# Performance work log

Hardware: AMD Instinct MI355X
Metric: run time of the kernel (lower is better)

## Reference

```python
import jax, jax.numpy as jnp
import numpy as np

B, S, D = 1, 2048, 2048
NH, NKV, HD = 16, 8, 128
FF = 8192
L = 2
V = 32000
THETA = 10000.0
EPS = 1e-5
SCALE = 0.02


def setup_inputs() -> dict:
    key = jax.random.key(0)
    ks = jax.random.split(key, 16)
    return {
        "input_ids": jax.random.randint(ks[0], (B, S), 0, V, dtype=jnp.int32),
        "embed": jax.random.normal(ks[1], (V, D), jnp.float32) * SCALE,
        "Wq": jax.random.normal(ks[2], (L, D, NH * HD), jnp.float32) * SCALE,
        "Wk": jax.random.normal(ks[3], (L, D, NKV * HD), jnp.float32) * SCALE,
        "Wv": jax.random.normal(ks[4], (L, D, NKV * HD), jnp.float32) * SCALE,
        "Wo": jax.random.normal(ks[5], (L, NH * HD, D), jnp.float32) * SCALE,
        "Wgate": jax.random.normal(ks[6], (L, D, FF), jnp.float32) * SCALE,
        "Wup": jax.random.normal(ks[7], (L, D, FF), jnp.float32) * SCALE,
        "Wdown": jax.random.normal(ks[8], (L, FF, D), jnp.float32) * SCALE,
        "norm_attn": jnp.ones((L, D), jnp.float32),
        "norm_mlp": jnp.ones((L, D), jnp.float32),
        "norm_final": jnp.ones((D,), jnp.float32),
        "lm_head": jax.random.normal(ks[9], (D, V), jnp.float32) * SCALE,
        "D1": jax.random.normal(ks[10], (S,), jnp.float32) + 2.0,
        "D2": jax.random.normal(ks[11], (HD,), jnp.float32) + 2.0,
        "D3": jax.random.normal(ks[12], (S,), jnp.float32) + 2.0,
    }


def _rms_norm(x, w):
    return x * jax.lax.rsqrt(jnp.mean(x * x, axis=-1, keepdims=True) + EPS) * w


def _rotate_half(x):
    x1, x2 = jnp.split(x, 2, axis=-1)
    return jnp.concatenate([-x2, x1], axis=-1)


def _forward(input_ids, embed, Wq, Wk, Wv, Wo, Wgate, Wup, Wdown,
             norm_attn, norm_mlp, norm_final, lm_head, D1, D2, D3):
    # RoPE tables: [1,1,S,HD]
    inv_freq = 1.0 / (THETA ** (jnp.arange(0, HD, 2, dtype=jnp.float32) / HD))
    freqs = jnp.arange(S, dtype=jnp.float32)[:, None] * inv_freq[None, :]
    emb = jnp.concatenate([freqs, freqs], axis=-1)
    cos = jnp.cos(emb)[None, None]
    sin = jnp.sin(emb)[None, None]
    causal = jnp.tril(jnp.ones((S, S), dtype=bool))
    neg = jnp.finfo(jnp.float32).min
    D1i, D2i, D3i = 1.0 / D1, 1.0 / D2, 1.0 / D3
    n_rep = NH // NKV

    h = embed[input_ids]  # [B,S,D]
    for l in range(L):
        # --- attention block ---
        x = _rms_norm(h, norm_attn[l])
        q = (x @ Wq[l]).reshape(B, S, NH, HD).transpose(0, 2, 1, 3)   # [B,NH,S,HD]
        k = (x @ Wk[l]).reshape(B, S, NKV, HD).transpose(0, 2, 1, 3)  # [B,NKV,S,HD]
        v = (x @ Wv[l]).reshape(B, S, NKV, HD).transpose(0, 2, 1, 3)
        q = q * cos + _rotate_half(q) * sin
        k = k * cos + _rotate_half(k) * sin
        # repeat_kv (GQA)
        k = jnp.repeat(k, n_rep, axis=1)
        v = jnp.repeat(v, n_rep, axis=1)
        # TEE diagonal encryption: Q' = D1 Q D2, K'^T = D2^-1 K^T D3
        q_enc = q * D1[None, None, :, None] * D2[None, None, None, :]
        k_enc = k * D3[None, None, :, None] * D2i[None, None, None, :]
        scores = jnp.einsum('bhqd,bhkd->bhqk', q_enc, k_enc)
        # decrypt: D1^-1 (Q'K'^T) D3^-1  (mathematically cancels encryption)
        scores = scores * D1i[None, None, :, None] * D3i[None, None, None, :]
        scores = scores / jnp.sqrt(jnp.float32(HD))
        scores = jnp.where(causal[None, None], scores, neg)
        probs = jax.nn.softmax(scores, axis=-1)
        o = jnp.einsum('bhqk,bhkd->bhqd', probs, v)
        o = o.transpose(0, 2, 1, 3).reshape(B, S, NH * HD)
        h = h + o @ Wo[l]
        # --- SwiGLU MLP block ---
        x = _rms_norm(h, norm_mlp[l])
        h = h + (jax.nn.silu(x @ Wgate[l]) * (x @ Wup[l])) @ Wdown[l]

    h = _rms_norm(h, norm_final)
    return h @ lm_head  # logits [B,S,V]


def reference(input_ids, embed, Wq, Wk, Wv, Wo, Wgate, Wup, Wdown,
              norm_attn, norm_mlp, norm_final, lm_head, D1, D2, D3):
    return _forward(input_ids, embed, Wq, Wk, Wv, Wo, Wgate, Wup, Wdown,
                    norm_attn, norm_mlp, norm_final, lm_head, D1, D2, D3)
```

## Files before the change

### kernel.cpp

```cpp
#include <hip/hip_runtime.h>
#include <cstdint>
#include <cstddef>

typedef __attribute__((ext_vector_type(4))) float f32x4;
typedef __attribute__((ext_vector_type(8))) short short8;
typedef __attribute__((ext_vector_type(4))) unsigned int u32x4;

static const int TS = 2048;
static const int DM = 2048;
static const int NHEAD = 16, NKVH = 8, HDIM = 128;
static const int FFD = 8192;
static const int NVOC = 32000;
static const int QKVN = 4096;

__device__ __forceinline__ unsigned short f2bf(float f){
  unsigned int u = __builtin_bit_cast(unsigned int, f);
  u += 0x7FFFu + ((u >> 16) & 1u);
  return (unsigned short)(u >> 16);
}
__device__ __forceinline__ float bf2f(short h){
  unsigned int u = ((unsigned int)(unsigned short)h) << 16;
  return __builtin_bit_cast(float, u);
}
__device__ __forceinline__ f32x4 mfma16(short8 a, short8 b, f32x4 c){
  return __builtin_amdgcn_mfma_f32_16x16x32_bf16(a, b, c, 0, 0, 0);
}
__device__ __forceinline__ void gload16(const void* g, void* l){
  __builtin_amdgcn_global_load_lds(
      (const __attribute__((address_space(1))) unsigned int*)g,
      (__attribute__((address_space(3))) unsigned int*)l, 16, 0, 0);
}
__device__ __forceinline__ long toff(int r, int k, int ldk){
  return ((long)((r >> 4) * ldk + (k >> 5)) << 9)
       + (((k & 31) >> 3) << 7) + ((r & 15) << 3) + (k & 7);
}

__global__ void rope_tables_k(float* __restrict__ cosT, float* __restrict__ sinT){
  int idx = blockIdx.x * 256 + threadIdx.x;
  int s = idx >> 6, j = idx & 63;
  float inv = exp2f(-(float)j * (13.287712379549449f / 64.0f));
  float ang = (float)s * inv;
  cosT[idx] = cosf(ang);
  sinT[idx] = sinf(ang);
}

__global__ void embed_k(const int* __restrict__ ids, const float* __restrict__ E,
                        float* __restrict__ h){
  int s = blockIdx.x, tid = threadIdx.x;
  long id = ids[s];
  const f32x4* src = (const f32x4*)(E + id * (long)DM);
  f32x4* dst = (f32x4*)(h + (long)s * DM);
  dst[tid] = src[tid];
  dst[tid + 256] = src[tid + 256];
}

__global__ void rmsnorm_k(const float* __restrict__ x, const float* __restrict__ w,
                          short* __restrict__ out){
  int s = blockIdx.x, tid = threadIdx.x;
  const float* row = x + (long)s * DM;
  f32x4 v0 = *(const f32x4*)&row[tid * 8];
  f32x4 v1 = *(const f32x4*)&row[tid * 8 + 4];
  float ss = v0[0]*v0[0] + v0[1]*v0[1] + v0[2]*v0[2] + v0[3]*v0[3]
           + v1[0]*v1[0] + v1[1]*v1[1] + v1[2]*v1[2] + v1[3]*v1[3];
  #pragma unroll
  for (int off = 32; off; off >>= 1) ss += __shfl_xor(ss, off);
  __shared__ float sred[4];
  int wave = tid >> 6, lane = tid & 63;
  if (lane == 0) sred[wave] = ss;
  __syncthreads();
  float tot = sred[0] + sred[1] + sred[2] + sred[3];
  float r = rsqrtf(tot * (1.0f / (float)DM) + 1e-5f);
  f32x4 w0 = *(const f32x4*)&w[tid * 8];
  f32x4 w1 = *(const f32x4*)&w[tid * 8 + 4];
  short8 o;
  #pragma unroll
  for (int j = 0; j < 4; j++) o[j] = (short)f2bf(v0[j] * r * w0[j]);
  #pragma unroll
  for (int j = 0; j < 4; j++) o[4 + j] = (short)f2bf(v1[j] * r * w1[j]);
  *(short8*)&out[toff(s, tid * 8, DM >> 5)] = o;
}

__global__ void reduce_rms_k(const float* __restrict__ p, float* __restrict__ h,
                             const float* __restrict__ w, short* __restrict__ out){
  const long stride = (long)TS * DM;
  int s = blockIdx.x, tid = threadIdx.x;
  long i = (long)s * DM + tid * 8;
  f32x4 a0 = *(const f32x4*)&h[i];
  f32x4 a1 = *(const f32x4*)&h[i + 4];
  {
    f32x4 v0 = *(const f32x4*)&p[i];
    f32x4 v1 = *(const f32x4*)&p[i + stride];
    f32x4 v2 = *(const f32x4*)&p[i + 2 * stride];
    f32x4 v3 = *(const f32x4*)&p[i + 3 * stride];
    a0 = a0 + ((v0 + v1) + (v2 + v3));
  }
  {
    f32x4 v0 = *(const f32x4*)&p[i + 4];
    f32x4 v1 = *(const f32x4*)&p[i + 4 + stride];
    f32x4 v2 = *(const f32x4*)&p[i + 4 + 2 * stride];
    f32x4 v3 = *(const f32x4*)&p[i + 4 + 3 * stride];
    a1 = a1 + ((v0 + v1) + (v2 + v3));
  }
  *(f32x4*)&h[i] = a0;
  *(f32x4*)&h[i + 4] = a1;
  float ss = a0[0]*a0[0] + a0[1]*a0[1] + a0[2]*a0[2] + a0[3]*a0[3]
           + a1[0]*a1[0] + a1[1]*a1[1] + a1[2]*a1[2] + a1[3]*a1[3];
  #pragma unroll
  for (int off = 32; off; off >>= 1) ss += __shfl_xor(ss, off);
  __shared__ float sred[4];
  int wave = tid >> 6, lane = tid & 63;
  if (lane == 0) sred[wave] = ss;
  __syncthreads();
  float tot = sred[0] + sred[1] + sred[2] + sred[3];
  float r = rsqrtf(tot * (1.0f / (float)DM) + 1e-5f);
  f32x4 w0 = *(const f32x4*)&w[tid * 8];
  f32x4 w1 = *(const f32x4*)&w[tid * 8 + 4];
  short8 o;
  #pragma unroll
  for (int j = 0; j < 4; j++) o[j] = (short)f2bf(a0[j] * r * w0[j]);
  #pragma unroll
  for (int j = 0; j < 4; j++) o[4 + j] = (short)f2bf(a1[j] * r * w1[j]);
  *(short8*)&out[toff(s, tid * 8, DM >> 5)] = o;
}

__global__ void transpose_k(const float* __restrict__ B, short* __restrict__ Bt,
                            int K, int N){
  __shared__ float t[64][65];
  int tid = threadIdx.x;
  int kb = blockIdx.y * 64, nb = blockIdx.x * 64;
  int r0 = tid >> 4, c4 = tid & 15;
  const int ldk = K >> 5;
  #pragma unroll
  for (int p = 0; p < 4; p++){
    int r = r0 + p * 16;
    f32x4 v = *(const f32x4*)&B[(long)(kb + r) * N + nb + c4 * 4];
    t[r][c4*4+0] = v[0]; t[r][c4*4+1] = v[1]; t[r][c4*4+2] = v[2]; t[r][c4*4+3] = v[3];
  }
  __syncthreads();
  int wave = tid >> 6, lane = tid & 63;
  #pragma unroll
  for (int p = 0; p < 2; p++){
    int s = wave * 2 + p;
    int rt = s >> 1, kt = s & 1;
    int n  = rt * 16 + (lane & 15);
    int k0 = kt * 32 + (lane >> 4) * 8;
    short8 o;
    #pragma unroll
    for (int j = 0; j < 8; j++) o[j] = (short)f2bf(t[k0 + j][n]);
    long base = (((long)((nb >> 4) + rt) * ldk + (kb >> 5) + kt) << 9);
    *(short8*)&Bt[base + lane * 8] = o;
  }
}

__global__ void vtrans_k(const short* __restrict__ vb, short* __restrict__ vtb, int stride){
  int s0 = blockIdx.x * 64, kv = blockIdx.y;
  int tid = threadIdx.x;
  int s = s0 + (tid & 63);
  int d0 = (tid >> 6) * 8;
  #pragma unroll
  for (int p = 0; p < 4; p++){
    int d = d0 + p * 32;
    short8 v = *(const short8*)&vb[(long)s * stride + kv * HDIM + d];
    #pragma unroll
    for (int j = 0; j < 8; j++)
      vtb[(long)(kv * HDIM + d + j) * TS + s] = v[j];
  }
}

__global__ void rope_apply_k(short* __restrict__ buf, const float* __restrict__ cosT,
                             const float* __restrict__ sinT, int nh, int stride, int coloff){
  int idx = blockIdx.x * 256 + threadIdx.x;
  int j = idx & 63;
  int t = idx >> 6;
  int hh = t % nh;
  int s = t / nh;
  long base = (long)s * stride + coloff + hh * HDIM + j;
  float c = cosT[s * 64 + j], sn = sinT[s * 64 + j];
  float x1 = bf2f(buf[base]), x2 = bf2f(buf[base + 64]);
  buf[base]      = (short)f2bf(x1 * c - x2 * sn);
  buf[base + 64] = (short)f2bf(x2 * c + x1 * sn);
}

template<int EPI>
__global__ __launch_bounds__(512, 2)
void gemm256(const short* __restrict__ A, int ldkA,
             const short* __restrict__ Bt, int ldkB,
             float* __restrict__ Cf, short* __restrict__ Cb,
             const short* __restrict__ Xtra, int N, int K, int ldkC){
  __shared__ short lds[4][2][8192];
  const int tid = threadIdx.x;
  const int wid = tid >> 6, lane = tid & 63;
  const int wr = wid >> 2, wc = wid & 3;
  const int fr = lane & 15, fch = lane >> 4;
  const int nt = K >> 5;

  const int z = blockIdx.y;
  const int k0 = z * nt;

  const int nbt = N >> 8;
  const int nwg = nbt << 3;
  const int q = nwg >> 3;
  const int swz = (blockIdx.x & 7) * q + (blockIdx.x >> 3);
  const int mb = swz & 7, nb = swz >> 3;

  const short* Abase = A  + ((long)(mb * 16) * ldkA + k0) * 512 + lane * 8;
  const short* Bbase = Bt + ((long)(nb * 16) * ldkB + k0) * 512 + lane * 8;
  const int gA0 = wid * 2, gA1 = wid * 2 + 1;

  short8 aE[4], aO[4], bE[2], bO[2];
  f32x4 acc[8][4] = {};

#define STG_A(bufc, g_, tau_) \
  gload16(Abase + ((long)(g_) * ldkA + (tau_)) * 512, &lds[bufc][0][(g_) * 512])
#define STG_B(bufc, g_, tau_) \
  gload16(Bbase + ((long)(g_) * ldkB + (tau_)) * 512, &lds[bufc][1][(g_) * 512])
#define RDA(dst, bufc, mh) do{ \
    _Pragma("unroll") \
    for (int j_ = 0; j_ < 4; j_++) \
      dst[j_] = *(const short8*)&lds[bufc][0][(wr * 8 + (mh) * 4 + j_) * 512 + fch * 128 + fr * 8]; \
  }while(0)
#define RDB(dst, bufc, nh) do{ \
    _Pragma("unroll") \
    for (int i_ = 0; i_ < 2; i_++) \
      dst[i_] = *(const short8*)&lds[bufc][1][(wc * 4 + (nh) * 2 + i_) * 512 + fch * 128 + fr * 8]; \
  }while(0)
#define MM8(va, vb, mh, nh) do{ \
    __builtin_amdgcn_s_setprio(1); \
    _Pragma("unroll") \
    for (int j_ = 0; j_ < 4; j_++) \
      _Pragma("unroll") \
      for (int i_ = 0; i_ < 2; i_++) \
        acc[(mh)*4+j_][(nh)*2+i_] = mfma16(va[j_], vb[i_], acc[(mh)*4+j_][(nh)*2+i_]); \
    __builtin_amdgcn_s_setprio(0); \
  }while(0)
#define SB __builtin_amdgcn_sched_barrier(0)

#define TILE(t_, bufR, bufN, bufS, bC, bNx) do{ \
    const int tau_ = ((t_) + 3 < nt) ? (t_) + 3 : nt - 1; \
    RDB(bNx, bufR, 1); STG_A(bufS, gA0, tau_); SB; MM8(aE, bC, 0, 0); \
    RDA(aO,  bufR, 1); STG_A(bufS, gA1, tau_); SB; MM8(aE, bNx, 0, 1); \
    asm volatile("s_waitcnt vmcnt(6)" ::: "memory"); \
    __builtin_amdgcn_s_barrier(); \
    RDA(aE,  bufN, 0); STG_B(bufS, gA0, tau_); SB; MM8(aO, bNx, 1, 1); \
    RDB(bNx, bufN, 0); STG_B(bufS, gA1, tau_); SB; MM8(aO, bC, 1, 0); \
    __builtin_amdgcn_s_barrier(); \
  }while(0)

  STG_A(0, gA0, 0); STG_A(0, gA1, 0); STG_B(0, gA0, 0); STG_B(0, gA1, 0);
  STG_A(1, gA0, 1); STG_A(1, gA1, 1); STG_B(1, gA0, 1); STG_B(1, gA1, 1);
  STG_A(2, gA0, 2); STG_A(2, gA1, 2); STG_B(2, gA0, 2); STG_B(2, gA1, 2);
  asm volatile("s_waitcnt vmcnt(8)" ::: "memory");
  __builtin_amdgcn_s_barrier();
  RDA(aE, 0, 0); RDB(bE, 0, 0);

  const int nIter = nt >> 2;
  for (int it = 0; it < nIter; ++it){
    const int t0 = it << 2;
    TILE(t0 + 0, 0, 1, 3, bE, bO);
    TILE(t0 + 1, 1, 2, 0, bO, bE);
    TILE(t0 + 2, 2, 3, 1, bE, bO);
    TILE(t0 + 3, 3, 0, 2, bO, bE);
  }
  asm volatile("s_waitcnt vmcnt(0)" ::: "memory");

#undef STG_A
#undef STG_B
#undef RDA
#undef RDB
#undef MM8
#undef SB
#undef TILE

  const int rb0 = mb * 256 + wr * 128 + fch * 4;
  const int cb0 = nb * 256 + wc * 64 + fr;
  const long pbase = (EPI == 5) ? (long)z * ((long)TS * N) : 0;
  #pragma unroll
  for (int m = 0; m < 8; m++)
    #pragma unroll
    for (int n = 0; n < 4; n++)
      #pragma unroll
      for (int i = 0; i < 4; i++){
        const int rr = rb0 + m * 16 + i, cc = cb0 + n * 16;
        long idx = (long)rr * N + cc;
        float v = acc[m][n][i];
        if constexpr (EPI == 1) Cb[idx] = (short)f2bf(v);
        else if constexpr (EPI == 3){
          float sg = 1.0f / (1.0f + __expf(-v));
          Cb[idx] = (short)f2bf(v * sg);
        } else if constexpr (EPI == 4){
          float g = bf2f(Xtra[idx]);
          Cb[toff(rr, cc, ldkC)] = (short)f2bf(g * v);
        } else {
          Cf[pbase + idx] = v;
        }
      }
}

__device__ __forceinline__ int qoff(int r, int cB){ return r * 256 + (cB ^ ((r & 7) << 4)); }
__device__ __forceinline__ int voff(int d, int cB){ return d * 128 + (cB ^ ((d & 7) << 4)); }
__device__ __forceinline__ int poff(int r, int cB){ return r * 128 + (cB ^ ((r & 7) << 4)); }

__global__ __launch_bounds__(256)
void attn_k(const short* __restrict__ qb, const short* __restrict__ kb,
            const short* __restrict__ vtb, short* __restrict__ ob){
  __shared__ short Qs[64 * 128];
  __shared__ short Ks[64 * 128];
  __shared__ short Vt[128 * 64];
  __shared__ short Ps[64 * 64];
  const int tid = threadIdx.x, wave = tid >> 6, lane = tid & 63;
  const int head = blockIdx.y, kvh = head >> 1;
  const int qt = (head & 8) ? (31 - blockIdx.x) : blockIdx.x;
  const float scale = 0.08838834764831845f;

  {
    int r0 = tid >> 4, c16 = tid & 15;
    #pragma unroll
    for (int p = 0; p < 4; p++){
      int r = r0 + p * 16;
      u32x4 v = *(const u32x4*)&qb[(long)(qt * 64 + r) * QKVN + head * HDIM + c16 * 8];
      *(u32x4*)((char*)Qs + qoff(r, c16 * 16)) = v;
    }
  }

  float mrun[4] = {-1e30f, -1e30f, -1e30f, -1e30f};
  float lrun[4] = {0.f, 0.f, 0.f, 0.f};
  f32x4 accO[8] = {};

  for (int kt = 0; kt <= qt; kt++){
    __syncthreads();
    {
      int r0 = tid >> 4, c16 = tid & 15;
      #pragma unroll
      for (int p = 0; p < 4; p++){
        int r = r0 + p * 16;
        u32x4 v = *(const u32x4*)&kb[(long)(kt * 64 + r) * QKVN + kvh * HDIM + c16 * 8];
        *(u32x4*)((char*)Ks + qoff(r, c16 * 16)) = v;
      }
      int vr0 = tid >> 3, vc = tid & 7;
      #pragma unroll
      for (int p = 0; p < 4; p++){
        int d = vr0 + p * 32;
        u32x4 v = *(const u32x4*)&vtb[(long)(kvh * HDIM + d) * TS + kt * 64 + vc * 8];
        *(u32x4*)((char*)Vt + voff(d, vc * 16)) = v;
      }
    }
    __syncthreads();

    f32x4 sacc[4] = {};
    #pragma unroll
    for (int k4 = 0; k4 < 4; k4++){
      short8 aq = *(const short8*)((const char*)Qs +
                   qoff(wave * 16 + (lane & 15), k4 * 64 + (lane >> 4) * 16));
      #pragma unroll
      for (int n = 0; n < 4; n++){
        short8 bk = *(const short8*)((const char*)Ks +
                     qoff(n * 16 + (lane & 15), k4 * 64 + (lane >> 4) * 16));
        sacc[n] = mfma16(aq, bk, sacc[n]);
      }
    }

    const bool diag = (kt == qt);
    float mt[4] = {-1e30f, -1e30f, -1e30f, -1e30f};
    #pragma unroll
    for (int n = 0; n < 4; n++)
      #pragma unroll
      for (int i = 0; i < 4; i++){
        float v = sacc[n][i] * scale;
        if (diag){
          int rr = (lane >> 4) * 4 + i + wave * 16;
          int cc = n * 16 + (lane & 15);
          if (cc > rr) v = -1e30f;
        }
        sacc[n][i] = v;
        mt[i] = fmaxf(mt[i], v);
      }
    #pragma unroll
    for (int off = 1; off < 16; off <<= 1)
      #pragma unroll
      for (int i = 0; i < 4; i++) mt[i] = fmaxf(mt[i], __shfl_xor(mt[i], off));
    float alpha[4], rsum[4];
    #pragma unroll
    for (int i = 0; i < 4; i++){
      float mn = fmaxf(mrun[i], mt[i]);
      alpha[i] = __expf(mrun[i] - mn);
      mrun[i] = mn;
      rsum[i] = 0.f;
    }
    #pragma unroll
    for (int n = 0; n < 4; n++)
      #pragma unroll
      for (int i = 0; i < 4; i++){
        float p = __expf(sacc[n][i] - mrun[i]);
        sacc[n][i] = p;
        rsum[i] += p;
      }
    #pragma unroll
    for (int off = 1; off < 16; off <<= 1)
      #pragma unroll
      for (int i = 0; i < 4; i++) rsum[i] += __shfl_xor(rsum[i], off);
    #pragma unroll
    for (int i = 0; i < 4; i++) lrun[i] = lrun[i] * alpha[i] + rsum[i];

    #pragma unroll
    for (int n = 0; n < 4; n++)
      #pragma unroll
      for (int i = 0; i < 4; i++){
        int rr = wave * 16 + (lane >> 4) * 4 + i;
        int cc = n * 16 + (lane & 15);
        *(short*)((char*)Ps + poff(rr, cc * 2)) = (short)f2bf(sacc[n][i]);
      }

    #pragma unroll
    for (int n = 0; n < 8; n++)
      #pragma unroll
      for (int i = 0; i < 4; i++) accO[n][i] *= alpha[i];
    #pragma unroll
    for (int ks = 0; ks < 2; ks++){
      short8 ap = *(const short8*)((const char*)Ps +
                   poff(wave * 16 + (lane & 15), ks * 64 + (lane >> 4) * 16));
      #pragma unroll
      for (int n = 0; n < 8; n++){
        short8 bv = *(const short8*)((const char*)Vt +
                     voff(n * 16 + (lane & 15), ks * 64 + (lane >> 4) * 16));
        accO[n] = mfma16(ap, bv, accO[n]);
      }
    }
  }

  #pragma unroll
  for (int i = 0; i < 4; i++){
    float inv = 1.0f / lrun[i];
    int rr = qt * 64 + wave * 16 + (lane >> 4) * 4 + i;
    #pragma unroll
    for (int n = 0; n < 8; n++){
      int cc = head * HDIM + n * 16 + (lane & 15);
      ob[toff(rr, cc, DM >> 5)] = (short)f2bf(accO[n][i] * inv);
    }
  }
}

extern "C" void kernel_launch(void* const* d_in, const int* in_sizes, int n_in,
                              void* d_out, int out_size, void* d_ws, size_t ws_size,
                              hipStream_t stream){
  (void)in_sizes; (void)n_in; (void)out_size; (void)ws_size;
  const int*   ids = (const int*)d_in[0];
  const float* E   = (const float*)d_in[1];
  const float* Wq  = (const float*)d_in[2];
  const float* Wk  = (const float*)d_in[3];
  const float* Wv  = (const float*)d_in[4];
  const float* Wo  = (const float*)d_in[5];
  const float* Wg  = (const float*)d_in[6];
  const float* Wu  = (const float*)d_in[7];
  const float* Wd  = (const float*)d_in[8];
  const float* nA  = (const float*)d_in[9];
  const float* nM  = (const float*)d_in[10];
  const float* nF  = (const float*)d_in[11];
  const float* LMH = (const float*)d_in[12];
  float* out = (float*)d_out;

  char* ws = (char*)d_ws;
  size_t off = 0;
  auto alloc = [&](size_t bytes){ void* p = ws + off; off += (bytes + 255) & ~(size_t)255; return p; };
  float* h    = (float*)alloc((size_t)TS * DM * 4);
  short* xb   = (short*)alloc((size_t)TS * DM * 2);
  short* qkvb = (short*)alloc((size_t)TS * QKVN * 2);
  short* vtb  = (short*)alloc((size_t)NKVH * HDIM * TS * 2);
  short* obuf = (short*)alloc((size_t)TS * DM * 2);
  short* sg   = (short*)alloc((size_t)TS * FFD * 2);
  short* actb = (short*)alloc((size_t)TS * FFD * 2);
  float* cosT = (float*)alloc((size_t)TS * 64 * 4);
  float* sinT = (float*)alloc((size_t)TS * 64 * 4);
  short* wT   = (short*)alloc((size_t)NVOC * DM * 2);
  float* pPart = (float*)((char*)wT + (size_t)36 * 1024 * 1024);

  rope_tables_k<<<512, 256, 0, stream>>>(cosT, sinT);
  embed_k<<<TS, 256, 0, stream>>>(ids, E, h);
  rmsnorm_k<<<TS, 256, 0, stream>>>(h, nA, xb);

  for (int l = 0; l < 2; l++){
    transpose_k<<<dim3(32, 32), 256, 0, stream>>>(Wq + (size_t)l * DM * DM, wT, DM, DM);
    transpose_k<<<dim3(16, 32), 256, 0, stream>>>(Wk + (size_t)l * DM * 1024, wT + (size_t)2048 * DM, DM, 1024);
    transpose_k<<<dim3(16, 32), 256, 0, stream>>>(Wv + (size_t)l * DM * 1024, wT + (size_t)3072 * DM, DM, 1024);
    gemm256<1><<<dim3(128), 512, 0, stream>>>(xb, 64, wT, 64, nullptr, qkvb, nullptr, QKVN, DM, 0);
    rope_apply_k<<<8192, 256, 0, stream>>>(qkvb, cosT, sinT, NHEAD, QKVN, 0);
    rope_apply_k<<<4096, 256, 0, stream>>>(qkvb, cosT, sinT, NKVH, QKVN, 2048);
    vtrans_k<<<dim3(32, 8), 256, 0, stream>>>(qkvb + 3072, vtb, QKVN);
    attn_k<<<dim3(32, 16), 256, 0, stream>>>(qkvb, qkvb + 2048, vtb, obuf);
    transpose_k<<<dim3(32, 32), 256, 0, stream>>>(Wo + (size_t)l * DM * DM, wT, DM, DM);
    gemm256<5><<<dim3(64, 4), 512, 0, stream>>>(obuf, 64, wT, 64, pPart, nullptr, nullptr, DM, DM / 4, 0);
    reduce_rms_k<<<TS, 256, 0, stream>>>(pPart, h, nM + (size_t)l * DM, xb);
    transpose_k<<<dim3(128, 32), 256, 0, stream>>>(Wg + (size_t)l * DM * FFD, wT, DM, FFD);
    gemm256<3><<<dim3(256), 512, 0, stream>>>(xb, 64, wT, 64, nullptr, sg, nullptr, FFD, DM, 0);
    transpose_k<<<dim3(128, 32), 256, 0, stream>>>(Wu + (size_t)l * DM * FFD, wT, DM, FFD);
    gemm256<4><<<dim3(256), 512, 0, stream>>>(xb, 64, wT, 64, nullptr, actb, sg, FFD, DM, FFD >> 5);
    transpose_k<<<dim3(32, 128), 256, 0, stream>>>(Wd + (size_t)l * FFD * DM, wT, FFD, DM);
    gemm256<5><<<dim3(64, 4), 512, 0, stream>>>(actb, 256, wT, 256, pPart, nullptr, nullptr, DM, FFD / 4, 0);
    if (l == 0)
      reduce_rms_k<<<TS, 256, 0, stream>>>(pPart, h, nA + (size_t)DM, xb);
    else
      reduce_rms_k<<<TS, 256, 0, stream>>>(pPart, h, nF, xb);
  }

  transpose_k<<<dim3(500, 32), 256, 0, stream>>>(LMH, wT, DM, NVOC);
  gemm256<0><<<dim3(1000), 512, 0, stream>>>(xb, 64, wT, 64, out, nullptr, nullptr, NVOC, DM, 0);
}
```

Baseline: 1.304 ms.

## Restructure GEMM main loop into double-buffered 64-wide K tiles

The 256x256 bf16 GEMM moves from a 4-stage ring of 32-wide K tiles to a 2-stage double buffer of 64-wide K tiles. The finely interleaved schedule with partial vmcnt waits and sched barriers is replaced by one prefetch per tile, then all LDS reads and MFMAs, then a full vmcnt(0) wait and a barrier. This halves the number of barriers per K step and simplifies the loop. In exchange the prefetch distance drops to one tile, and the full drain of outstanding global loads each tile can leave the MFMA units waiting on memory. The epilogue also gets an explicit branch for the split-K output path, which does not change behaviour.

New measurement: 1.304 ms. About the same (+0.0%).

```diff
diff --git a/kernel.cpp b/kernel.cpp
--- a/kernel.cpp
+++ b/kernel.cpp
@@ -187,15 +187,15 @@
              const short* __restrict__ Bt, int ldkB,
              float* __restrict__ Cf, short* __restrict__ Cb,
              const short* __restrict__ Xtra, int N, int K, int ldkC){
-  __shared__ short lds[4][2][8192];
+  __shared__ short lds[2][2][16384];
   const int tid = threadIdx.x;
   const int wid = tid >> 6, lane = tid & 63;
   const int wr = wid >> 2, wc = wid & 3;
   const int fr = lane & 15, fch = lane >> 4;
-  const int nt = K >> 5;
+  const int nt2 = K >> 6;
 
   const int z = blockIdx.y;
-  const int k0 = z * nt;
+  const int k0 = z * (K >> 5);
 
   const int nbt = N >> 8;
   const int nwg = nbt << 3;
@@ -210,19 +210,26 @@
   short8 aE[4], aO[4], bE[2], bO[2];
   f32x4 acc[8][4] = {};
 
-#define STG_A(bufc, g_, tau_) \
-  gload16(Abase + ((long)(g_) * ldkA + (tau_)) * 512, &lds[bufc][0][(g_) * 512])
-#define STG_B(bufc, g_, tau_) \
-  gload16(Bbase + ((long)(g_) * ldkB + (tau_)) * 512, &lds[bufc][1][(g_) * 512])
-#define RDA(dst, bufc, mh) do{ \
+#define STG64(bufc, tt) do{ \
+    const int t2_ = (tt) * 2; \
+    gload16(Abase + ((long)gA0 * ldkA + t2_    ) * 512, &lds[bufc][0][(gA0 * 2 + 0) * 512]); \
+    gload16(Abase + ((long)gA0 * ldkA + t2_ + 1) * 512, &lds[bufc][0][(gA0 * 2 + 1) * 512]); \
+    gload16(Abase + ((long)gA1 * ldkA + t2_    ) * 512, &lds[bufc][0][(gA1 * 2 + 0) * 512]); \
+    gload16(Abase + ((long)gA1 * ldkA + t2_ + 1) * 512, &lds[bufc][0][(gA1 * 2 + 1) * 512]); \
+    gload16(Bbase + ((long)gA0 * ldkB + t2_    ) * 512, &lds[bufc][1][(gA0 * 2 + 0) * 512]); \
+    gload16(Bbase + ((long)gA0 * ldkB + t2_ + 1) * 512, &lds[bufc][1][(gA0 * 2 + 1) * 512]); \
+    gload16(Bbase + ((long)gA1 * ldkB + t2_    ) * 512, &lds[bufc][1][(gA1 * 2 + 0) * 512]); \
+    gload16(Bbase + ((long)gA1 * ldkB + t2_ + 1) * 512, &lds[bufc][1][(gA1 * 2 + 1) * 512]); \
+  }while(0)
+#define RDA64(dst, bufc, mh, kt) do{ \
     _Pragma("unroll") \
     for (int j_ = 0; j_ < 4; j_++) \
-      dst[j_] = *(const short8*)&lds[bufc][0][(wr * 8 + (mh) * 4 + j_) * 512 + fch * 128 + fr * 8]; \
+      dst[j_] = *(const short8*)&lds[bufc][0][(((wr * 8 + (mh) * 4 + j_) * 2) + (kt)) * 512 + fch * 128 + fr * 8]; \
   }while(0)
-#define RDB(dst, bufc, nh) do{ \
+#define RDB64(dst, bufc, nh, kt) do{ \
     _Pragma("unroll") \
     for (int i_ = 0; i_ < 2; i_++) \
-      dst[i_] = *(const short8*)&lds[bufc][1][(wc * 4 + (nh) * 2 + i_) * 512 + fch * 128 + fr * 8]; \
+      dst[i_] = *(const short8*)&lds[bufc][1][(((wc * 4 + (nh) * 2 + i_) * 2) + (kt)) * 512 + fch * 128 + fr * 8]; \
   }while(0)
 #define MM8(va, vb, mh, nh) do{ \
     __builtin_amdgcn_s_setprio(1); \
@@ -233,43 +240,34 @@
         acc[(mh)*4+j_][(nh)*2+i_] = mfma16(va[j_], vb[i_], acc[(mh)*4+j_][(nh)*2+i_]); \
     __builtin_amdgcn_s_setprio(0); \
   }while(0)
-#define SB __builtin_amdgcn_sched_barrier(0)
-
-#define TILE(t_, bufR, bufN, bufS, bC, bNx) do{ \
-    const int tau_ = ((t_) + 3 < nt) ? (t_) + 3 : nt - 1; \
-    RDB(bNx, bufR, 1); STG_A(bufS, gA0, tau_); SB; MM8(aE, bC, 0, 0); \
-    RDA(aO,  bufR, 1); STG_A(bufS, gA1, tau_); SB; MM8(aE, bNx, 0, 1); \
-    asm volatile("s_waitcnt vmcnt(6)" ::: "memory"); \
-    __builtin_amdgcn_s_barrier(); \
-    RDA(aE,  bufN, 0); STG_B(bufS, gA0, tau_); SB; MM8(aO, bNx, 1, 1); \
-    RDB(bNx, bufN, 0); STG_B(bufS, gA1, tau_); SB; MM8(aO, bC, 1, 0); \
+
+#define TILE64(t_, bufR, bufS) do{ \
+    const int ts_ = ((t_) + 1 < nt2) ? (t_) + 1 : (t_); \
+    STG64(bufS, ts_); \
+    RDA64(aE, bufR, 0, 0); RDB64(bE, bufR, 0, 0); MM8(aE, bE, 0, 0); \
+    RDB64(bO, bufR, 1, 0); MM8(aE, bO, 0, 1); \
+    RDA64(aO, bufR, 1, 0); MM8(aO, bO, 1, 1); MM8(aO, bE, 1, 0); \
+    RDA64(aE, bufR, 0, 1); RDB64(bE, bufR, 0, 1); MM8(aE, bE, 0, 0); \
+    RDB64(bO, bufR, 1, 1); MM8(aE, bO, 0, 1); \
+    RDA64(aO, bufR, 1, 1); MM8(aO, bO, 1, 1); MM8(aO, bE, 1, 0); \
+    asm volatile("s_waitcnt vmcnt(0)" ::: "memory"); \
     __builtin_amdgcn_s_barrier(); \
   }while(0)
 
-  STG_A(0, gA0, 0); STG_A(0, gA1, 0); STG_B(0, gA0, 0); STG_B(0, gA1, 0);
-  STG_A(1, gA0, 1); STG_A(1, gA1, 1); STG_B(1, gA0, 1); STG_B(1, gA1, 1);
-  STG_A(2, gA0, 2); STG_A(2, gA1, 2); STG_B(2, gA0, 2); STG_B(2, gA1, 2);
-  asm volatile("s_waitcnt vmcnt(8)" ::: "memory");
+  STG64(0, 0);
+  asm volatile("s_waitcnt vmcnt(0)" ::: "memory");
   __builtin_amdgcn_s_barrier();
-  RDA(aE, 0, 0); RDB(bE, 0, 0);
-
-  const int nIter = nt >> 2;
-  for (int it = 0; it < nIter; ++it){
-    const int t0 = it << 2;
-    TILE(t0 + 0, 0, 1, 3, bE, bO);
-    TILE(t0 + 1, 1, 2, 0, bO, bE);
-    TILE(t0 + 2, 2, 3, 1, bE, bO);
-    TILE(t0 + 3, 3, 0, 2, bO, bE);
-  }
-  asm volatile("s_waitcnt vmcnt(0)" ::: "memory");
-
-#undef STG_A
-#undef STG_B
-#undef RDA
-#undef RDB
+
+  for (int it = 0; it < nt2; it += 2){
+    TILE64(it,     0, 1);
+    TILE64(it + 1, 1, 0);
+  }
+
+#undef STG64
+#undef RDA64
+#undef RDB64
 #undef MM8
-#undef SB
-#undef TILE
+#undef TILE64
 
   const int rb0 = mb * 256 + wr * 128 + fch * 4;
   const int cb0 = nb * 256 + wc * 64 + fr;
@@ -290,8 +288,10 @@
         } else if constexpr (EPI == 4){
           float g = bf2f(Xtra[idx]);
           Cb[toff(rr, cc, ldkC)] = (short)f2bf(g * v);
+        } else if constexpr (EPI == 5){
+          Cf[pbase + idx] = v;
         } else {
-          Cf[pbase + idx] = v;
+          Cf[idx] = v;
         }
       }
 }
```
